# Performance work log

Measured on AMD Instinct MI355X. Metric: run time of the kernel, lower is better.

Reference implementation:

```python
import jax, jax.numpy as jnp
import numpy as np

V, D, B, NEG = 100000, 128, 4096, 5
D_INNER = int(D * 2.0 * 2 / 3)  # nGPT FF inner dim = 170

def l2norm(t, axis=-1):
    return t / jnp.linalg.norm(t, axis=axis, keepdims=True)

def setup_inputs() -> dict:
    key = jax.random.key(0)
    ks = jax.random.split(key, 8)
    return {
        "input_ids": jax.random.randint(ks[0], (B,), 0, V),
        "target_ids": jax.random.randint(ks[1], (B,), 0, V),
        "neg_ids": jax.random.randint(ks[2], (B, NEG), 0, V),
        "W_in": jax.random.normal(ks[3], (V, D), jnp.float32) * (1.0 / np.sqrt(D)),
        "W_out": jax.random.normal(ks[4], (V, D), jnp.float32) * (1.0 / np.sqrt(D)),
        "W_hidden": jax.random.normal(ks[5], (D_INNER, D), jnp.float32) * 0.02,
        "W_gate": jax.random.normal(ks[6], (D_INNER, D), jnp.float32) * 0.02,
        "W_ff_out": jax.random.normal(ks[7], (D, D_INNER), jnp.float32) * 0.02,
        "hidden_scale": jnp.ones((D_INNER,), jnp.float32),
        "gate_scale": jnp.ones((D_INNER,), jnp.float32),
        "logit_scale": jnp.full((V,), D ** -0.5, dtype=jnp.float32),  # Scale param init = s_logit_scale
    }

def reference(input_ids, target_ids, neg_ids, W_in, W_out, W_hidden, W_gate,
              W_ff_out, hidden_scale, gate_scale, logit_scale):
    # skipgram: gather normalized input embeddings
    emb = l2norm(W_in)[input_ids]                                  # (B, D)
    # nGPT FeedForward: silu-gated, weights l2-normalized on input dim
    h = (emb @ l2norm(W_hidden).T) * hidden_scale                  # (B, D_INNER)
    g = (emb @ l2norm(W_gate).T) * gate_scale * jnp.sqrt(jnp.float32(D))
    x = jax.nn.silu(g) * h
    x = x @ l2norm(W_ff_out, axis=0).T                             # (B, D), to_out norm_dim_in=False
    # logits over full vocab, scaled by Scale(): param * (init/scale)
    scale_eff = logit_scale * (1.0 / (D ** -0.5))                  # (V,)
    logits = (x @ l2norm(W_out).T) * scale_eff                     # (B, V)
    # negative-sampling loss: gather positive + sampled negative logits
    pos = jnp.take_along_axis(logits, target_ids[:, None], axis=1)  # (B, 1)
    neg = jnp.take_along_axis(logits, neg_ids, axis=1)              # (B, NEG)
    positive_loss = jax.nn.log_sigmoid(pos).mean()
    negative_loss = jax.nn.log_sigmoid(-neg).mean()
    return -(positive_loss + negative_loss)
```

## Files before the change

kernel.cpp:

```cpp
#include <hip/hip_runtime.h>
#include <math.h>

#define DD    128
#define DI    170
#define DIP   176
#define ND4   32
#define NI4   43
#define BB    4096
#define NNEG  5
#define ROWS  8
#define NBLK  (BB / ROWS)
#define NTHR  512
#define SQRT_D 11.3137084989847603904f

#define WS_WHT 0
#define WS_WGT (ND4 * DIP * 4)
#define WS_WFT (2 * ND4 * DIP * 4)

__device__ __forceinline__ float wave_bcast_sum(float v) {
#pragma unroll
    for (int m = 1; m < 64; m <<= 1) v += __shfl_xor(v, m, 64);
    return v;
}

__global__ __launch_bounds__(256) void prep_kernel(
    const float* __restrict__ W_hidden,
    const float* __restrict__ W_gate,
    const float* __restrict__ W_ff_out,
    const float* __restrict__ hidden_scale,
    const float* __restrict__ gate_scale,
    float* __restrict__ ws,
    float* __restrict__ out)
{
    if (blockIdx.x == 0 && threadIdx.x == 0) out[0] = 0.0f;
    const int wave = threadIdx.x >> 6;
    const int lane = threadIdx.x & 63;
    const int t = blockIdx.x * 4 + wave;
    float* whT = ws + WS_WHT;
    float* wgT = ws + WS_WGT;
    float* wfT = ws + WS_WFT;

    if (t < DI) {
        const int v = t;
        float a = W_ff_out[(long)(2 * lane)     * DI + v];
        float b = W_ff_out[(long)(2 * lane + 1) * DI + v];
        float cf = wave_bcast_sum(a * a + b * b);
        float2 ph = ((const float2*)(W_hidden + (long)v * DD))[lane];
        float2 pg = ((const float2*)(W_gate   + (long)v * DD))[lane];
        float sh = wave_bcast_sum(ph.x * ph.x + ph.y * ph.y);
        float sg = wave_bcast_sum(pg.x * pg.x + pg.y * pg.y);
        const float whs = rsqrtf(sh) * hidden_scale[v] * rsqrtf(cf);
        const float wgs = rsqrtf(sg) * gate_scale[v] * SQRT_D;
        const int d4   = lane >> 1;
        const int half = lane & 1;
        float2* dh = (float2*)(whT + ((long)d4 * DIP + v) * 4 + half * 2);
        *dh = make_float2(ph.x * whs, ph.y * whs);
        float2* dg = (float2*)(wgT + ((long)d4 * DIP + v) * 4 + half * 2);
        *dg = make_float2(pg.x * wgs, pg.y * wgs);
    } else if (t < DI + NI4) {
        const int i4 = t - DI;
#pragma unroll
        for (int rr = 0; rr < 2; ++rr) {
            const int dd = rr * 64 + lane;
            float4 v4;
            if (i4 < 42) {
                float2 lo = *(const float2*)(W_ff_out + (long)dd * DI + 4 * i4);
                float2 hi = *(const float2*)(W_ff_out + (long)dd * DI + 4 * i4 + 2);
                v4 = make_float4(lo.x, lo.y, hi.x, hi.y);
            } else {
                float2 lo = *(const float2*)(W_ff_out + (long)dd * DI + 168);
                v4 = make_float4(lo.x, lo.y, 0.0f, 0.0f);
            }
            *(float4*)(wfT + ((long)i4 * DD + dd) * 4) = v4;
        }
    } else if (t == DI + NI4 || t == DI + NI4 + 1) {
        float* base = (t == DI + NI4) ? whT : wgT;
        for (int idx = lane; idx < ND4 * 6; idx += 64) {
            const int d4 = idx / 6, c = idx % 6;
            *(float4*)(base + ((long)d4 * DIP + DI + c) * 4) =
                make_float4(0.0f, 0.0f, 0.0f, 0.0f);
        }
    }
}

__global__ __launch_bounds__(NTHR, 4) void main_kernel(
    const int*   __restrict__ input_ids,
    const int*   __restrict__ target_ids,
    const int*   __restrict__ neg_ids,
    const float* __restrict__ W_in,
    const float* __restrict__ W_out,
    const float* __restrict__ logit_scale,
    const float* __restrict__ ws,
    float* __restrict__ out)
{
    __shared__ __align__(16) float s_emb[ROWS][DD];
    __shared__ __align__(16) float s_x[ROWS][DIP];
    __shared__ __align__(16) float s_xout[ROWS][DD];
    __shared__ float s_partg[DIP][9];
    __shared__ float s_red[8];

    const int tid  = threadIdx.x;
    const int wave = tid >> 6;
    const int lane = tid & 63;
    const int b0   = blockIdx.x * ROWS;

    const float4* whT4 = (const float4*)(ws + WS_WHT);
    const float4* wgT4 = (const float4*)(ws + WS_WGT);
    const float4* wfT4 = (const float4*)(ws + WS_WFT);

    {
        const int id = input_ids[b0 + wave];
        float2 p = ((const float2*)(W_in + (long)id * DD))[lane];
        float s  = wave_bcast_sum(p.x * p.x + p.y * p.y);
        float inv = rsqrtf(s);
        s_emb[wave][2 * lane]     = p.x * inv;
        s_emb[wave][2 * lane + 1] = p.y * inv;
    }
    __syncthreads();

    const bool g0 = (tid < DIP);
    const bool g1 = (tid >= 256 && tid < 256 + DIP);
    float a[ROWS];
#pragma unroll
    for (int r = 0; r < ROWS; ++r) a[r] = 0.0f;
    const int i = g0 ? tid : (g1 ? tid - 256 : -1);

    if (i >= 0) {
        const float4* wT = g0 ? whT4 : wgT4;
#pragma unroll 4
        for (int d4 = 0; d4 < ND4; ++d4) {
            float4 w4 = wT[d4 * DIP + i];
#pragma unroll
            for (int r = 0; r < ROWS; ++r) {
                float4 e4 = ((const float4*)s_emb[r])[d4];
                a[r] += e4.x * w4.x + e4.y * w4.y + e4.z * w4.z + e4.w * w4.w;
            }
        }
    }
    if (g1) {
#pragma unroll
        for (int r = 0; r < ROWS; ++r) s_partg[i][r] = a[r];
    }
    __syncthreads();

    if (g0) {
#pragma unroll
        for (int r = 0; r < ROWS; ++r) {
            float h = a[r];
            float g = s_partg[i][r];
            float x = (g / (1.0f + __expf(-g))) * h;
            s_x[r][i] = x;
        }
    }
    __syncthreads();

    {
        const int dd = tid & 127;
        const int r0 = tid >> 7;
        float acc0 = 0.0f, acc1 = 0.0f;
#pragma unroll 4
        for (int i4 = 0; i4 < NI4; ++i4) {
            float4 w4 = wfT4[i4 * DD + dd];
            float4 xa = ((const float4*)s_x[r0])[i4];
            float4 xb = ((const float4*)s_x[r0 + 4])[i4];
            acc0 += w4.x * xa.x + w4.y * xa.y + w4.z * xa.z + w4.w * xa.w;
            acc1 += w4.x * xb.x + w4.y * xb.y + w4.z * xb.z + w4.w * xb.w;
        }
        s_xout[r0][dd]     = acc0;
        s_xout[r0 + 4][dd] = acc1;
    }
    __syncthreads();

    float wacc = 0.0f;
    for (int t = wave; t < ROWS * (1 + NNEG); t += 8) {
        const int r  = t / (1 + NNEG);
        const int jj = t % (1 + NNEG);
        const int bidx = b0 + r;
        const int id = (jj == 0) ? target_ids[bidx] : neg_ids[bidx * NNEG + jj - 1];
        const float* wrow = W_out + (long)id * DD;
        float w0 = wrow[lane], w1 = wrow[64 + lane];
        float x0 = s_xout[r][lane], x1 = s_xout[r][64 + lane];
        float dot = w0 * x0 + w1 * x1;
        float ss  = w0 * w0 + w1 * w1;
#pragma unroll
        for (int m = 1; m < 64; m <<= 1) {
            dot += __shfl_xor(dot, m, 64);
            ss  += __shfl_xor(ss,  m, 64);
        }
        const float logit = dot * rsqrtf(ss) * logit_scale[id] * SQRT_D;
        const float z  = (jj == 0) ? logit : -logit;
        const float ls = fminf(z, 0.0f) - log1pf(__expf(-fabsf(z)));
        wacc += (jj == 0) ? ls * (1.0f / BB) : ls * (1.0f / (BB * NNEG));
    }
    if (lane == 0) s_red[wave] = wacc;
    __syncthreads();
    if (tid == 0) {
        float tot = s_red[0] + s_red[1] + s_red[2] + s_red[3]
                  + s_red[4] + s_red[5] + s_red[6] + s_red[7];
        atomicAdd(out, -tot);
    }
}

extern "C" void kernel_launch(void* const* d_in, const int* in_sizes, int n_in,
                              void* d_out, int out_size, void* d_ws, size_t ws_size,
                              hipStream_t stream) {
    (void)in_sizes; (void)n_in; (void)out_size; (void)ws_size;
    const int*   input_ids    = (const int*)  d_in[0];
    const int*   target_ids   = (const int*)  d_in[1];
    const int*   neg_ids      = (const int*)  d_in[2];
    const float* W_in         = (const float*)d_in[3];
    const float* W_out        = (const float*)d_in[4];
    const float* W_hidden     = (const float*)d_in[5];
    const float* W_gate       = (const float*)d_in[6];
    const float* W_ff_out     = (const float*)d_in[7];
    const float* hidden_scale = (const float*)d_in[8];
    const float* gate_scale   = (const float*)d_in[9];
    const float* logit_scale  = (const float*)d_in[10];
    float* out = (float*)d_out;
    float* ws  = (float*)d_ws;

    prep_kernel<<<54, 256, 0, stream>>>(W_hidden, W_gate, W_ff_out,
                                        hidden_scale, gate_scale, ws, out);
    main_kernel<<<NBLK, NTHR, 0, stream>>>(input_ids, target_ids, neg_ids,
                                           W_in, W_out, logit_scale, ws, out);
}
```

Baseline: 160.1 us.

## Halve rows per block and split the FF output matmul across thread quarters

Each block now handles 4 batch rows instead of 8, which doubles the block count, and launch bounds now request higher occupancy. The FF output projection is split along the inner dimension into four chunks of 11 float4 each, one per 128-thread quarter. Partial sums are reduced through a new shared buffer, and the ff_out weight is zero-padded to 44 float4 chunks. This aims for more parallelism and latency hiding, at the cost of re-reading the FF weights twice as often per batch row and adding an extra barrier.

```diff
diff --git a/kernel.cpp b/kernel.cpp
--- a/kernel.cpp
+++ b/kernel.cpp
@@ -5,10 +5,10 @@
 #define DI    170
 #define DIP   176
 #define ND4   32
-#define NI4   43
+#define NI4P  44
 #define BB    4096
 #define NNEG  5
-#define ROWS  8
+#define ROWS  4
 #define NBLK  (BB / ROWS)
 #define NTHR  512
 #define SQRT_D 11.3137084989847603904f
@@ -57,7 +57,7 @@
         *dh = make_float2(ph.x * whs, ph.y * whs);
         float2* dg = (float2*)(wgT + ((long)d4 * DIP + v) * 4 + half * 2);
         *dg = make_float2(pg.x * wgs, pg.y * wgs);
-    } else if (t < DI + NI4) {
+    } else if (t < DI + NI4P) {
         const int i4 = t - DI;
 #pragma unroll
         for (int rr = 0; rr < 2; ++rr) {
@@ -67,14 +67,16 @@
                 float2 lo = *(const float2*)(W_ff_out + (long)dd * DI + 4 * i4);
                 float2 hi = *(const float2*)(W_ff_out + (long)dd * DI + 4 * i4 + 2);
                 v4 = make_float4(lo.x, lo.y, hi.x, hi.y);
-            } else {
+            } else if (i4 == 42) {
                 float2 lo = *(const float2*)(W_ff_out + (long)dd * DI + 168);
                 v4 = make_float4(lo.x, lo.y, 0.0f, 0.0f);
+            } else {
+                v4 = make_float4(0.0f, 0.0f, 0.0f, 0.0f);
             }
             *(float4*)(wfT + ((long)i4 * DD + dd) * 4) = v4;
         }
-    } else if (t == DI + NI4 || t == DI + NI4 + 1) {
-        float* base = (t == DI + NI4) ? whT : wgT;
+    } else if (t == DI + NI4P || t == DI + NI4P + 1) {
+        float* base = (t == DI + NI4P) ? whT : wgT;
         for (int idx = lane; idx < ND4 * 6; idx += 64) {
             const int d4 = idx / 6, c = idx % 6;
             *(float4*)(base + ((long)d4 * DIP + DI + c) * 4) =
@@ -83,7 +85,7 @@
     }
 }
 
-__global__ __launch_bounds__(NTHR, 4) void main_kernel(
+__global__ __launch_bounds__(NTHR, 8) void main_kernel(
     const int*   __restrict__ input_ids,
     const int*   __restrict__ target_ids,
     const int*   __restrict__ neg_ids,
@@ -96,7 +98,8 @@
     __shared__ __align__(16) float s_emb[ROWS][DD];
     __shared__ __align__(16) float s_x[ROWS][DIP];
     __shared__ __align__(16) float s_xout[ROWS][DD];
-    __shared__ float s_partg[DIP][9];
+    __shared__ __align__(16) float s_pp[4][ROWS][DD];
+    __shared__ float s_partg[DIP][ROWS + 1];
     __shared__ float s_red[8];
 
     const int tid  = threadIdx.x;
@@ -108,7 +111,7 @@
     const float4* wgT4 = (const float4*)(ws + WS_WGT);
     const float4* wfT4 = (const float4*)(ws + WS_WFT);
 
-    {
+    if (wave < ROWS) {
         const int id = input_ids[b0 + wave];
         float2 p = ((const float2*)(W_in + (long)id * DD))[lane];
         float s  = wave_bcast_sum(p.x * p.x + p.y * p.y);
@@ -156,18 +159,30 @@
 
     {
         const int dd = tid & 127;
-        const int r0 = tid >> 7;
-        float acc0 = 0.0f, acc1 = 0.0f;
+        const int q  = tid >> 7;
+        float acc[ROWS];
+#pragma unroll
+        for (int r = 0; r < ROWS; ++r) acc[r] = 0.0f;
+        const int i4lo = q * 11;
 #pragma unroll 4
-        for (int i4 = 0; i4 < NI4; ++i4) {
+        for (int k = 0; k < 11; ++k) {
+            const int i4 = i4lo + k;
             float4 w4 = wfT4[i4 * DD + dd];
-            float4 xa = ((const float4*)s_x[r0])[i4];
-            float4 xb = ((const float4*)s_x[r0 + 4])[i4];
-            acc0 += w4.x * xa.x + w4.y * xa.y + w4.z * xa.z + w4.w * xa.w;
-            acc1 += w4.x * xb.x + w4.y * xb.y + w4.z * xb.z + w4.w * xb.w;
-        }
-        s_xout[r0][dd]     = acc0;
-        s_xout[r0 + 4][dd] = acc1;
+#pragma unroll
+            for (int r = 0; r < ROWS; ++r) {
+                float4 x4 = ((const float4*)s_x[r])[i4];
+                acc[r] += w4.x * x4.x + w4.y * x4.y + w4.z * x4.z + w4.w * x4.w;
+            }
+        }
+#pragma unroll
+        for (int r = 0; r < ROWS; ++r) s_pp[q][r][dd] = acc[r];
+    }
+    __syncthreads();
+    {
+        const int dd = tid & 127;
+        const int r  = tid >> 7;
+        float v = ((s_pp[0][r][dd] + s_pp[1][r][dd]) + s_pp[2][r][dd]) + s_pp[3][r][dd];
+        s_xout[r][dd] = v;
     }
     __syncthreads();
 
```

New measurement: 155.9 us. 1.03x faster.
